# Kernel tuning notes

Measured on AMD Instinct MI355X. Metric: run time of the kernel, lower is better.

## Reference

```python
import jax, jax.numpy as jnp
import numpy as np

B, L, D, N, NL = 8, 32768, 64, 16, 4


def setup_inputs() -> dict:
    key = jax.random.key(0)
    ks = jax.random.split(key, 32)
    r = lambda i, shape, s=1.0: s * jax.random.normal(ks[i], shape, dtype=jnp.float32)
    return {
        "inputs": r(0, (B, L)),
        "w_init": r(1, (D, 1), 0.5), "b_init": r(2, (D,), 0.1),
        "s4_ln_w": 1.0 + r(3, (NL, D), 0.05), "s4_ln_b": r(4, (NL, D), 0.05),
        "log_dt": r(5, (NL, D), 0.5) - 4.0,          # dt ~ exp(-4) ~ 0.018
        "log_A_real": r(6, (NL, D, N), 0.3),
        "A_imag": r(7, (NL, D, N)),
        "C_re": r(8, (NL, D, N), 0.5), "C_im": r(9, (NL, D, N), 0.5),
        "D_skip": r(10, (NL, D)),
        "s4_out_w": r(11, (NL, 2 * D, D), 0.1), "s4_out_b": r(12, (NL, 2 * D), 0.05),
        "ff_ln_w": 1.0 + r(13, (NL, D), 0.05), "ff_ln_b": r(14, (NL, D), 0.05),
        "ff_w1": r(15, (NL, 2 * D, D), 0.1), "ff_b1": r(16, (NL, 2 * D), 0.05),
        "ff_w2": r(17, (NL, D, 2 * D), 0.1), "ff_b2": r(18, (NL, D), 0.05),
        "norm_w": 1.0 + r(19, (D,), 0.05), "norm_b": r(20, (D,), 0.05),
        "w_final1": r(21, (D, D), 0.1), "b_final1": r(22, (D,), 0.05),
        "w_zero": r(23, (1, D), 0.02), "b_zero": r(24, (1,), 0.01),
    }


def _ln(x, w, b):
    # layernorm over channel dim of [B, D, L] (TransposedLN)
    m = jnp.mean(x, axis=1, keepdims=True)
    v = jnp.var(x, axis=1, keepdims=True)
    return (x - m) * jax.lax.rsqrt(v + 1e-5) * w[None, :, None] + b[None, :, None]


def _s4d(z, log_dt, log_A_real, A_imag, C_re, C_im, D_skip):
    # S4D (diagonal SSM) with ZOH discretization; z: [B, D, L]
    Lq = z.shape[-1]
    dt = jnp.exp(log_dt)                              # [D]
    A = -jnp.exp(log_A_real) + 1j * A_imag            # [D, N]
    dtA = A * dt[:, None]                             # [D, N]
    C = (C_re + 1j * C_im) * (jnp.exp(dtA) - 1.0) / A # dC = C * (e^{dtA}-1)/A
    t = jnp.arange(Lq)
    # Vandermonde kernel K[d, l] = 2 Re sum_n dC[d,n] e^{dtA[d,n] * l}
    K = 2.0 * jnp.real(jnp.einsum('dn,dnl->dl', C, jnp.exp(dtA[:, :, None] * t)))
    n = 2 * Lq
    y = jnp.fft.irfft(jnp.fft.rfft(z, n) * jnp.fft.rfft(K, n)[None], n)[..., :Lq]
    return y + D_skip[None, :, None] * z


def reference(inputs, w_init, b_init, s4_ln_w, s4_ln_b, log_dt, log_A_real,
              A_imag, C_re, C_im, D_skip, s4_out_w, s4_out_b, ff_ln_w, ff_ln_b,
              ff_w1, ff_b1, ff_w2, ff_b2, norm_w, norm_b, w_final1, b_final1,
              w_zero, b_zero):
    # init conv (1x1) + ReLU; inputs [B, L] -> x [B, D, L]
    x = jax.nn.relu(jnp.einsum('dc,bcl->bdl', w_init, inputs[:, None, :])
                    + b_init[None, :, None])
    for i in range(NL):
        # --- S4 residual block: LN -> S4D -> GELU -> 1x1 conv to 2D -> GLU ---
        z = _ln(x, s4_ln_w[i], s4_ln_b[i])
        y = _s4d(z, log_dt[i], log_A_real[i], A_imag[i], C_re[i], C_im[i], D_skip[i])
        y = jax.nn.gelu(y)
        u = jnp.einsum('ed,bdl->bel', s4_out_w[i], y) + s4_out_b[i][None, :, None]
        a, g = jnp.split(u, 2, axis=1)
        x = x + a * jax.nn.sigmoid(g)
        z = _ln(x, ff_ln_w[i], ff_ln_b[i])
        h = jax.nn.gelu(jnp.einsum('ed,bdl->bel', ff_w1[i], z) + ff_b1[i][None, :, None])
        x = x + jnp.einsum('de,bel->bdl', ff_w2[i], h) + ff_b2[i][None, :, None]
    # final norm + conv head
    x = _ln(x, norm_w, norm_b)
    x = jax.nn.relu(jnp.einsum('ed,bdl->bel', w_final1, x) + b_final1[None, :, None])
    x = jnp.einsum('od,bdl->bol', w_zero, x) + b_zero[None, :, None]
    return x[:, 0, :]  # squeeze out_channels=1 -> [B, L]
```

## Files before the change

### kernel.cpp

```cpp
#include <hip/hip_runtime.h>
#include <cmath>

constexpr int Bq = 8, Lq = 32768, Dq = 64, Nq = 16, NLq = 4;
constexpr int CLq = 128, NCq = 256;
constexpr int PT = Bq * Lq / 16;

typedef _Float16 f16;
typedef _Float16 half2t __attribute__((ext_vector_type(2)));
typedef _Float16 half4 __attribute__((ext_vector_type(4)));
typedef _Float16 half8 __attribute__((ext_vector_type(8)));
typedef float f32x4 __attribute__((ext_vector_type(4)));
typedef float f32x2 __attribute__((ext_vector_type(2)));

static __device__ __forceinline__ float sigm(float x) { return 1.0f / (1.0f + __expf(-x)); }
static __device__ __forceinline__ float gelu_t(float x) {
  return x * sigm(1.5957691216057308f * fmaf(0.044715f * x * x, x, x));
}

__global__ __launch_bounds__(128) void k_wtall(
    const float* __restrict__ log_dt, const float* __restrict__ log_A_real,
    const float* __restrict__ A_imag, const float* __restrict__ C_re,
    const float* __restrict__ C_im, const float* __restrict__ dskip,
    f32x2* __restrict__ LCL, f32x2* __restrict__ LC2K, half8* __restrict__ TF,
    half8* __restrict__ VF, half8* __restrict__ WF) {
  __shared__ f32x2 pw[129][16];
  __shared__ f32x2 lamS[16], dcS[16];
  __shared__ float Ks[128];
  int d = blockIdx.x & 63, L = blockIdx.x >> 6;
  half8* TFl = TF + (size_t)L * 131072;
  half8* VFl = VF + (size_t)L * 32768;
  half8* WFl = WF + (size_t)L * 32768;
  int t = threadIdx.x;
  if (t < 16) {
    int di = L * 64 + d;
    int idx = di * 16 + t;
    float dt = expf(log_dt[di]);
    float Ar = -expf(log_A_real[idx]);
    float Ai = A_imag[idx];
    float dr = Ar * dt, dmi = Ai * dt;
    float er = expf(dr);
    float lr = er * cosf(dmi), li = er * sinf(dmi);
    float inv = 1.0f / (Ar * Ar + Ai * Ai);
    float e1r = lr - 1.0f, e1i = li;
    float qr = (e1r * Ar + e1i * Ai) * inv;
    float qi = (e1i * Ar - e1r * Ai) * inv;
    float cr = C_re[idx], ci = C_im[idx];
    lamS[t] = f32x2{lr, li};
    dcS[t] = f32x2{2.0f * (cr * qr - ci * qi), 2.0f * (cr * qi + ci * qr)};
    float erc = expf(dr * 128.0f);
    f32x2 l128 = f32x2{erc * cosf(dmi * 128.0f), erc * sinf(dmi * 128.0f)};
    pw[128][t] = l128;
    LCL[(size_t)L * 1024 + d * 16 + t] = l128;
    float br = l128.x, bi = l128.y;
#pragma unroll
    for (int q = 0; q < 4; q++) {
      float t2 = br * br - bi * bi;
      bi = 2.f * br * bi; br = t2;
    }
    LC2K[(size_t)L * 1024 + d * 16 + t] = f32x2{br, bi};
  }
  __syncthreads();
#pragma unroll
  for (int n = 0; n < 16; n++) {
    f32x2 lam = lamS[n];
    float pr = 1.f, pi = 0.f, br = lam.x, bi = lam.y;
    int e = t;
    while (e) {
      if (e & 1) { float tt = pr * br - pi * bi; pi = fmaf(pr, bi, pi * br); pr = tt; }
      float t2 = br * br - bi * bi; bi = 2.f * br * bi; br = t2; e >>= 1;
    }
    pw[t][n] = f32x2{pr, pi};
  }
  __syncthreads();
  {
    float k = 0.f;
#pragma unroll
    for (int n = 0; n < 16; n++) {
      f32x2 dc = dcS[n];
      f32x2 p = pw[t][n];
      k += dc.x * p.x - dc.y * p.y;
    }
    if (t == 0) k += dskip[L * 64 + d];
    Ks[t] = k;
  }
  __syncthreads();
  for (int s = t; s < 2048; s += 128) {
    int ln = s & 63, kt = (s >> 6) & 3, mt = s >> 8;
    int jo = mt * 16 + (ln & 15);
    int ji0 = kt * 32 + (ln >> 4) * 8;
    half8 v;
#pragma unroll
    for (int jj = 0; jj < 8; jj++) {
      int ji = ji0 + jj;
      v[jj] = (jo >= ji) ? (f16)Ks[jo - ji] : (f16)0.f;
    }
    TFl[(size_t)d * 2048 + s] = v;
  }
  for (int s = t; s < 512; s += 128) {
    int ln = s & 63, mt = s >> 6;
    int jo = mt * 16 + (ln & 15);
    int q0 = (ln >> 4) * 8;
    half8 v;
#pragma unroll
    for (int jj = 0; jj < 8; jj++) {
      int q = q0 + jj, n = q >> 1;
      f32x2 dc = dcS[n];
      f32x2 p = pw[jo + 1][n];
      float wr = dc.x * p.x - dc.y * p.y;
      float wi = dc.x * p.y + dc.y * p.x;
      v[jj] = (q & 1) ? (f16)(-wi) : (f16)wr;
    }
    VFl[(size_t)d * 512 + s] = v;
  }
  for (int s = t; s < 512; s += 128) {
    int ln = s & 63, kt = (s >> 6) & 3, nt = s >> 8;
    int p_ = nt * 16 + (ln & 15);
    int n = p_ >> 1;
    int j0 = kt * 32 + (ln >> 4) * 8;
    half8 v;
#pragma unroll
    for (int jj = 0; jj < 8; jj++) {
      f32x2 p = pw[127 - (j0 + jj)][n];
      v[jj] = (p_ & 1) ? (f16)p.y : (f16)p.x;
    }
    WFl[(size_t)d * 512 + s] = v;
  }
}

__global__ __launch_bounds__(512) void k_init3(
    const float* __restrict__ inp, const float* __restrict__ w_init,
    const float* __restrict__ b_init, const float* __restrict__ lnw,
    const float* __restrict__ lnb, f16* __restrict__ X, f16* __restrict__ Z16) {
  __shared__ __align__(16) f16 ztile[64 * 132];
  int tid = threadIdx.x;
  int widx = tid >> 6, lane = tid & 63;
  int pl = lane & 15, qh = lane >> 4;
  for (int k = 0; k < 4; ++k) {
    int pt = blockIdx.x * 8 + widx + k * 4096;
    int pos = pt * 16 + pl;
    float v = inp[pos];
    float s = 0.f, s2 = 0.f;
    f32x4 o[4];
#pragma unroll
    for (int q = 0; q < 4; q++) {
      int d0 = q * 16 + qh * 4;
      f32x4 w4 = *(const f32x4*)(w_init + d0);
      f32x4 b4 = *(const f32x4*)(b_init + d0);
#pragma unroll
      for (int j = 0; j < 4; j++) {
        float t = fmaf(w4[j], v, b4[j]);
        t = t > 0.f ? t : 0.f;
        o[q][j] = t; s += t; s2 += t * t;
      }
      half4 xo = half4{(f16)o[q][0], (f16)o[q][1], (f16)o[q][2], (f16)o[q][3]};
      *(half4*)(X + (size_t)pos * 64 + d0) = xo;
    }
    s += __shfl_xor(s, 16); s += __shfl_xor(s, 32);
    s2 += __shfl_xor(s2, 16); s2 += __shfl_xor(s2, 32);
    float m = s * (1.0f / 64.0f);
    float rstd = rsqrtf(s2 * (1.0f / 64.0f) - m * m + 1e-5f);
    int prow = widx * 16 + pl;
#pragma unroll
    for (int q = 0; q < 4; q++) {
      int d0 = q * 16 + qh * 4;
      f32x4 lw = *(const f32x4*)(lnw + d0);
      f32x4 lb = *(const f32x4*)(lnb + d0);
#pragma unroll
      for (int r = 0; r < 4; r++)
        ztile[(d0 + r) * 132 + prow] = (f16)fmaf((o[q][r] - m) * rstd, lw[r], lb[r]);
    }
    __syncthreads();
    {
      int d = tid >> 3, c0 = (tid & 7) * 16;
      half8 z0 = *(const half8*)(ztile + d * 132 + c0);
      half8 z1 = *(const half8*)(ztile + d * 132 + c0 + 8);
      size_t zoff = (size_t)d * 262144 + (size_t)(blockIdx.x * 8 + k * 4096) * 16;
      *(half8*)(Z16 + zoff + c0) = z0;
      *(half8*)(Z16 + zoff + c0 + 8) = z1;
    }
    __syncthreads();
  }
}

__global__ __launch_bounds__(256) void k_p1g(
    const f16* __restrict__ Z16, const half8* __restrict__ WF, f16* __restrict__ S16) {
  int tid = threadIdx.x;
  int lane = tid & 63;
  int task = blockIdx.x * 4 + (tid >> 6);
  int d = task >> 7, bct = task & 127;
  int bc0 = bct * 16;
  int pl = lane & 15, qh = lane >> 4;
  half8 az[4];
  const f16* zp = Z16 + ((size_t)d * 2048 + bc0 + pl) * 128 + qh * 8;
#pragma unroll
  for (int kt = 0; kt < 4; kt++) az[kt] = *(const half8*)(zp + kt * 32);
#pragma unroll
  for (int nt = 0; nt < 2; nt++) {
    f32x4 acc = f32x4{0.f, 0.f, 0.f, 0.f};
#pragma unroll
    for (int kt = 0; kt < 4; kt++)
      acc = __builtin_amdgcn_mfma_f32_16x16x32_f16(az[kt], WF[(size_t)d * 512 + (nt * 4 + kt) * 64 + lane], acc, 0, 0, 0);
#pragma unroll
    for (int r = 0; r < 4; r++)
      S16[((size_t)d * 2048 + bc0 + qh * 4 + r) * 32 + nt * 16 + pl] = (f16)acc[r];
  }
}

__global__ __launch_bounds__(256) void k_pass2(
    const f16* __restrict__ S16, const f32x2* __restrict__ LCLl,
    const f32x2* __restrict__ LC2Kl, f16* __restrict__ Sc) {
  __shared__ f32x2 gc[16][17];
  int blk = blockIdx.x;
  int d = blk >> 3, b = blk & 7;
  int t = threadIdx.x;
  int n = t & 15, g = t >> 4;
  f32x2 lam = LCLl[d * 16 + n];
  size_t base = ((size_t)d * 2048 + b * 256 + g * 16) * 32 + 2 * n;
  const f16* sp = S16 + base;
  float cr = 0.f, ci = 0.f;
#pragma unroll 4
  for (int j = 0; j < 16; j++) {
    half2t v = *(const half2t*)(sp + (size_t)j * 32);
    float nr = fmaf(lam.x, cr, fmaf(-lam.y, ci, (float)v[0]));
    float ni = fmaf(lam.x, ci, fmaf(lam.y, cr, (float)v[1]));
    cr = nr; ci = ni;
  }
  gc[g][n] = f32x2{cr, ci};
  __syncthreads();
  f32x2 l2 = LC2Kl[d * 16 + n];
  float er = 0.f, ei = 0.f;
  for (int gg = 0; gg < g; gg++) {
    f32x2 c = gc[gg][n];
    float nr = fmaf(l2.x, er, fmaf(-l2.y, ei, c.x));
    float ni = fmaf(l2.x, ei, fmaf(l2.y, er, c.y));
    er = nr; ei = ni;
  }
  f16* cp = Sc + base;
  float cr2 = er, ci2 = ei;
#pragma unroll 4
  for (int j = 0; j < 16; j++) {
    *(half2t*)(cp + (size_t)j * 32) = half2t{(f16)cr2, (f16)ci2};
    half2t v = *(const half2t*)(sp + (size_t)j * 32);
    float nr = fmaf(lam.x, cr2, fmaf(-lam.y, ci2, (float)v[0]));
    float ni = fmaf(lam.x, ci2, fmaf(lam.y, cr2, (float)v[1]));
    cr2 = nr; ci2 = ni;
  }
}

__global__ __launch_bounds__(256) void k_p3g2(
    const f16* __restrict__ Z16, const f16* __restrict__ Sc,
    const half8* __restrict__ TF, const half8* __restrict__ VF,
    f16* __restrict__ Y16) {
  int tid = threadIdx.x;
  int lane = tid & 63, widx = tid >> 6;
  int bct = blockIdx.x & 127, dg = blockIdx.x >> 7;
  int bc0 = bct * 16;
  int dbase = dg * 16 + widx * 4;
  int pl = lane & 15, qh = lane >> 4;
  half8 zb[4][4];
  half8 sb[4];
#pragma unroll
  for (int di = 0; di < 4; di++) {
    int d = dbase + di;
    const f16* zp = Z16 + ((size_t)d * 2048 + bc0 + pl) * 128 + qh * 8;
#pragma unroll
    for (int kt = 0; kt < 4; kt++) zb[di][kt] = *(const half8*)(zp + kt * 32);
    sb[di] = *(const half8*)(Sc + ((size_t)d * 2048 + bc0 + pl) * 32 + qh * 8);
  }
#pragma unroll
  for (int mt = 0; mt < 8; mt++) {
    const int KTM = mt / 2 + 1;
    f32x4 acc[4];
#pragma unroll
    for (int di = 0; di < 4; di++) {
      int d = dbase + di;
      acc[di] = f32x4{0.f, 0.f, 0.f, 0.f};
      const half8* tfp = TF + ((size_t)d * 8 + mt) * 256 + lane;
#pragma unroll
      for (int kt = 0; kt < KTM; kt++)
        acc[di] = __builtin_amdgcn_mfma_f32_16x16x32_f16(tfp[kt * 64], zb[di][kt], acc[di], 0, 0, 0);
      acc[di] = __builtin_amdgcn_mfma_f32_16x16x32_f16(VF[((size_t)d * 8 + mt) * 64 + lane], sb[di], acc[di], 0, 0, 0);
    }
#pragma unroll
    for (int r = 0; r < 4; r++) {
      int pos = (bc0 + pl) * 128 + mt * 16 + qh * 4 + r;
      half4 pk = half4{(f16)gelu_t(acc[0][r]), (f16)gelu_t(acc[1][r]),
                       (f16)gelu_t(acc[2][r]), (f16)gelu_t(acc[3][r])};
      *(half4*)(Y16 + (size_t)pos * 64 + dbase) = pk;
    }
  }
}

template <int WZ>
__global__ __launch_bounds__(512) void k_gluff3(
    const f16* __restrict__ Y16, const float* __restrict__ Wg, const float* __restrict__ bg,
    const float* __restrict__ W1, const float* __restrict__ b1,
    const float* __restrict__ W2, const float* __restrict__ b2,
    const float* __restrict__ lnw, const float* __restrict__ lnb,
    const float* __restrict__ nlnw, const float* __restrict__ nlnb,
    f16* __restrict__ X, f16* __restrict__ Z16,
    const float* __restrict__ Wf, const float* __restrict__ bfb,
    const float* __restrict__ wz, const float* __restrict__ bz,
    float* __restrict__ outp) {
  __shared__ __align__(16) char smem[68352];
  int tid = threadIdx.x;
#pragma unroll
  for (int it = 0; it < 2; it++) {
    int s = it * 512 + tid;
    int l = s & 63, ks = (s >> 6) & 1, et = s >> 7;
    const float* wp = Wg + (et * 16 + (l & 15)) * 64 + ks * 32 + (l >> 4) * 8;
    f32x4 w0 = *(const f32x4*)wp, w1 = *(const f32x4*)(wp + 4);
    *(half8*)(smem + s * 16) = half8{(f16)w0[0], (f16)w0[1], (f16)w0[2], (f16)w0[3],
                                     (f16)w1[0], (f16)w1[1], (f16)w1[2], (f16)w1[3]};
  }
#pragma unroll
  for (int it = 0; it < 2; it++) {
    int s = it * 512 + tid;
    int l = s & 63, ks = (s >> 6) & 1, et = s >> 7;
    int pls = l & 15, qhs = l >> 4;
    const float* wp = W1 + (et * 16 + pls) * 64 + ks * 32 + qhs * 4;
    f32x4 w0 = *(const f32x4*)wp;
    f32x4 w1 = *(const f32x4*)(wp + 16);
    *(half8*)(smem + 16384 + s * 16) = half8{(f16)w0[0], (f16)w0[1], (f16)w0[2], (f16)w0[3],
                                             (f16)w1[0], (f16)w1[1], (f16)w1[2], (f16)w1[3]};
  }
#pragma unroll
  for (int it = 0; it < 2; it++) {
    int s = it * 512 + tid;
    int l = s & 63, ks = (s >> 6) & 3, dt = s >> 8;
    int pls = l & 15, qhs = l >> 4;
    const float* wp = W2 + (dt * 16 + pls) * 128 + ks * 32 + qhs * 4;
    f32x4 w0 = *(const f32x4*)wp;
    f32x4 w1 = *(const f32x4*)(wp + 16);
    *(half8*)(smem + 32768 + s * 16) = half8{(f16)w0[0], (f16)w0[1], (f16)w0[2], (f16)w0[3],
                                             (f16)w1[0], (f16)w1[1], (f16)w1[2], (f16)w1[3]};
  }
  for (int idx = tid; idx < 576; idx += 512) {
    float v;
    if (idx < 128) v = bg[idx];
    else if (idx < 256) v = b1[idx - 128];
    else if (idx < 320) v = b2[idx - 256];
    else if (idx < 384) v = lnw[idx - 320];
    else if (idx < 448) v = lnb[idx - 384];
    else if (idx < 512) v = nlnw[idx - 448];
    else v = nlnb[idx - 512];
    ((float*)(smem + 49152))[idx] = v;
  }
  if constexpr (!WZ) {
    if (tid < 512) {
      int s = tid;
      int l = s & 63, ks = (s >> 6) & 1, et = s >> 7;
      int pls = l & 15, qhs = l >> 4;
      const float* wp = Wf + (et * 16 + pls) * 64 + ks * 32 + qhs * 4;
      f32x4 w0 = *(const f32x4*)wp;
      f32x4 w1 = *(const f32x4*)(wp + 16);
      *(half8*)(smem + 51456 + s * 16) = half8{(f16)w0[0], (f16)w0[1], (f16)w0[2], (f16)w0[3],
                                               (f16)w1[0], (f16)w1[1], (f16)w1[2], (f16)w1[3]};
    }
    if (tid < 129) {
      float v = tid < 64 ? bfb[tid] : (tid < 128 ? wz[tid - 64] : bz[0]);
      ((float*)(smem + 59648))[tid] = v;
    }
  }
  __syncthreads();
  int lane = tid & 63, pl = lane & 15, qh = lane >> 4;
  int widx = tid >> 6;
  f16* ztile = (f16*)(smem + 51456);

  for (int k = 0; k < 4; ++k) {
    int pt = blockIdx.x * 8 + widx + k * 4096;
    int pos = pt * 16 + pl;
    half8 yb0 = *(const half8*)(Y16 + (size_t)pos * 64 + qh * 8);
    half8 yb1 = *(const half8*)(Y16 + (size_t)pos * 64 + 32 + qh * 8);
    f32x4 xv[4];
#pragma unroll
    for (int q = 0; q < 4; q++) {
      half4 xh = *(const half4*)(X + (size_t)pos * 64 + q * 16 + qh * 4);
#pragma unroll
      for (int r = 0; r < 4; r++) xv[q][r] = (float)xh[r];
    }

    unsigned sb = 0;
    asm volatile("" : "+v"(sb));
    const char* sm = smem + sb;
    const half8* sWg = (const half8*)sm;
    const half8* sW1 = (const half8*)(sm + 16384);
    const half8* sW2 = (const half8*)(sm + 32768);
    const float* sf = (const float*)(sm + 49152);
    f32x4 accg[8];
#pragma unroll
    for (int et = 0; et < 8; et++) accg[et] = *(const f32x4*)(sf + et * 16 + qh * 4);
#pragma unroll
    for (int et = 0; et < 8; et++)
      accg[et] = __builtin_amdgcn_mfma_f32_16x16x32_f16(sWg[(et * 2) * 64 + lane], yb0, accg[et], 0, 0, 0);
#pragma unroll
    for (int et = 0; et < 8; et++)
      accg[et] = __builtin_amdgcn_mfma_f32_16x16x32_f16(sWg[(et * 2 + 1) * 64 + lane], yb1, accg[et], 0, 0, 0);
    float s = 0.f, s2 = 0.f;
#pragma unroll
    for (int q = 0; q < 4; q++)
#pragma unroll
      for (int r = 0; r < 4; r++) {
        xv[q][r] += accg[q][r] * sigm(accg[q + 4][r]);
        s += xv[q][r]; s2 += xv[q][r] * xv[q][r];
      }
    s += __shfl_xor(s, 16); s += __shfl_xor(s, 32);
    s2 += __shfl_xor(s2, 16); s2 += __shfl_xor(s2, 32);
    float m = s * (1.0f / 64.0f);
    float rstd = rsqrtf(s2 * (1.0f / 64.0f) - m * m + 1e-5f);
    half4 zb4[4];
#pragma unroll
    for (int ks = 0; ks < 4; ks++) {
      f32x4 lw = *(const f32x4*)(sf + 320 + ks * 16 + qh * 4);
      f32x4 lb = *(const f32x4*)(sf + 384 + ks * 16 + qh * 4);
      half4 z;
#pragma unroll
      for (int r = 0; r < 4; r++) z[r] = (f16)fmaf((xv[ks][r] - m) * rstd, lw[r], lb[r]);
      zb4[ks] = z;
    }
    f32x4 acc1[8];
#pragma unroll
    for (int et = 0; et < 8; et++) acc1[et] = *(const f32x4*)(sf + 128 + et * 16 + qh * 4);
#pragma unroll
    for (int ks = 0; ks < 2; ks++) {
      half4 a = zb4[ks * 2], b = zb4[ks * 2 + 1];
      half8 zb8 = half8{a[0], a[1], a[2], a[3], b[0], b[1], b[2], b[3]};
#pragma unroll
      for (int et = 0; et < 8; et++)
        acc1[et] = __builtin_amdgcn_mfma_f32_16x16x32_f16(sW1[(et * 2 + ks) * 64 + lane], zb8, acc1[et], 0, 0, 0);
    }
    half4 h4[8];
#pragma unroll
    for (int et = 0; et < 8; et++)
      h4[et] = half4{(f16)gelu_t(acc1[et][0]), (f16)gelu_t(acc1[et][1]),
                     (f16)gelu_t(acc1[et][2]), (f16)gelu_t(acc1[et][3])};
    f32x4 acc2[4];
#pragma unroll
    for (int dt = 0; dt < 4; dt++) acc2[dt] = *(const f32x4*)(sf + 256 + dt * 16 + qh * 4);
#pragma unroll
    for (int ks = 0; ks < 4; ks++) {
      half4 a = h4[ks * 2], b = h4[ks * 2 + 1];
      half8 hb8 = half8{a[0], a[1], a[2], a[3], b[0], b[1], b[2], b[3]};
#pragma unroll
      for (int dt = 0; dt < 4; dt++)
        acc2[dt] = __builtin_amdgcn_mfma_f32_16x16x32_f16(sW2[(dt * 4 + ks) * 64 + lane], hb8, acc2[dt], 0, 0, 0);
    }
    s = 0.f; s2 = 0.f;
#pragma unroll
    for (int dt = 0; dt < 4; dt++) {
#pragma unroll
      for (int r = 0; r < 4; r++) {
        xv[dt][r] += acc2[dt][r];
        s += xv[dt][r]; s2 += xv[dt][r] * xv[dt][r];
      }
      if constexpr (WZ) {
        half4 xo = half4{(f16)xv[dt][0], (f16)xv[dt][1], (f16)xv[dt][2], (f16)xv[dt][3]};
        *(half4*)(X + (size_t)pos * 64 + dt * 16 + qh * 4) = xo;
      }
    }
    s += __shfl_xor(s, 16); s += __shfl_xor(s, 32);
    s2 += __shfl_xor(s2, 16); s2 += __shfl_xor(s2, 32);
    float m2 = s * (1.0f / 64.0f);
    float rstd2 = rsqrtf(s2 * (1.0f / 64.0f) - m2 * m2 + 1e-5f);

    if constexpr (WZ) {
      int prow = widx * 16 + pl;
#pragma unroll
      for (int q = 0; q < 4; q++) {
        int d0 = q * 16 + qh * 4;
        f32x4 lw = *(const f32x4*)(sf + 448 + d0);
        f32x4 lb = *(const f32x4*)(sf + 512 + d0);
#pragma unroll
        for (int r = 0; r < 4; r++)
          ztile[(d0 + r) * 132 + prow] = (f16)fmaf((xv[q][r] - m2) * rstd2, lw[r], lb[r]);
      }
      __syncthreads();
      {
        int d = tid >> 3, c0 = (tid & 7) * 16;
        half8 z0 = *(const half8*)(ztile + d * 132 + c0);
        half8 z1 = *(const half8*)(ztile + d * 132 + c0 + 8);
        size_t zoff = (size_t)d * 262144 + (size_t)(blockIdx.x * 8 + k * 4096) * 16;
        *(half8*)(Z16 + zoff + c0) = z0;
        *(half8*)(Z16 + zoff + c0 + 8) = z1;
      }
      __syncthreads();
    } else {
      const half8* sWf = (const half8*)(sm + 51456);
      const float* hf = (const float*)(sm + 59648);
      half4 hz[4];
#pragma unroll
      for (int ks = 0; ks < 4; ks++) {
        f32x4 lw = *(const f32x4*)(sf + 448 + ks * 16 + qh * 4);
        f32x4 lb = *(const f32x4*)(sf + 512 + ks * 16 + qh * 4);
        half4 z;
#pragma unroll
        for (int r = 0; r < 4; r++) z[r] = (f16)fmaf((xv[ks][r] - m2) * rstd2, lw[r], lb[r]);
        hz[ks] = z;
      }
      f32x4 acch[4];
#pragma unroll
      for (int et = 0; et < 4; et++) acch[et] = *(const f32x4*)(hf + et * 16 + qh * 4);
#pragma unroll
      for (int ks = 0; ks < 2; ks++) {
        half4 a = hz[ks * 2], b = hz[ks * 2 + 1];
        half8 zb8 = half8{a[0], a[1], a[2], a[3], b[0], b[1], b[2], b[3]};
#pragma unroll
        for (int et = 0; et < 4; et++)
          acch[et] = __builtin_amdgcn_mfma_f32_16x16x32_f16(sWf[(et * 2 + ks) * 64 + lane], zb8, acch[et], 0, 0, 0);
      }
      float o = 0.f;
#pragma unroll
      for (int et = 0; et < 4; et++) {
        f32x4 wzv = *(const f32x4*)(hf + 64 + et * 16 + qh * 4);
#pragma unroll
        for (int r = 0; r < 4; r++) {
          float rv = acch[et][r];
          rv = rv > 0.f ? rv : 0.f;
          o = fmaf(wzv[r], rv, o);
        }
      }
      o += __shfl_xor(o, 16); o += __shfl_xor(o, 32);
      if (qh == 0) outp[pos] = o + hf[128];
    }
  }
}

extern "C" void kernel_launch(void* const* d_in, const int* in_sizes, int n_in,
                              void* d_out, int out_size, void* d_ws, size_t ws_size,
                              hipStream_t stream) {
  (void)in_sizes; (void)n_in; (void)out_size; (void)ws_size;
  const float* inputs   = (const float*)d_in[0];
  const float* w_init   = (const float*)d_in[1];
  const float* b_init   = (const float*)d_in[2];
  const float* s4_ln_w  = (const float*)d_in[3];
  const float* s4_ln_b  = (const float*)d_in[4];
  const float* log_dt   = (const float*)d_in[5];
  const float* log_A    = (const float*)d_in[6];
  const float* A_imag   = (const float*)d_in[7];
  const float* C_re     = (const float*)d_in[8];
  const float* C_im     = (const float*)d_in[9];
  const float* D_skip   = (const float*)d_in[10];
  const float* s4_out_w = (const float*)d_in[11];
  const float* s4_out_b = (const float*)d_in[12];
  const float* ff_ln_w  = (const float*)d_in[13];
  const float* ff_ln_b  = (const float*)d_in[14];
  const float* ff_w1    = (const float*)d_in[15];
  const float* ff_b1    = (const float*)d_in[16];
  const float* ff_w2    = (const float*)d_in[17];
  const float* ff_b2    = (const float*)d_in[18];
  const float* norm_w   = (const float*)d_in[19];
  const float* norm_b   = (const float*)d_in[20];
  const float* w_final1 = (const float*)d_in[21];
  const float* b_final1 = (const float*)d_in[22];
  const float* w_zero   = (const float*)d_in[23];
  const float* b_zero   = (const float*)d_in[24];

  char* w8 = (char*)d_ws;
  size_t off = 0;
  f16*   X     = (f16*)(w8 + off);   off += (size_t)33554432;
  f16*   Z16   = (f16*)(w8 + off);   off += (size_t)33554432;
  f16*   Y16   = (f16*)(w8 + off);   off += (size_t)33554432;
  f16*   S16   = (f16*)(w8 + off);   off += (size_t)8388608;
  f16*   Sc    = (f16*)(w8 + off);   off += (size_t)8388608;
  f32x2* LCL   = (f32x2*)(w8 + off); off += 32768;
  f32x2* LC2K  = (f32x2*)(w8 + off); off += 32768;
  half8* TF    = (half8*)(w8 + off); off += (size_t)8388608;
  half8* VF    = (half8*)(w8 + off); off += (size_t)2097152;
  half8* WF    = (half8*)(w8 + off); off += (size_t)2097152;

  k_wtall<<<256, 128, 0, stream>>>(log_dt, log_A, A_imag, C_re, C_im, D_skip,
                                   LCL, LC2K, TF, VF, WF);
  k_init3<<<512, 512, 0, stream>>>(inputs, w_init, b_init, s4_ln_w, s4_ln_b, X, Z16);
  for (int i = 0; i < NLq; i++) {
    k_p1g<<<2048, 256, 0, stream>>>(Z16, WF + (size_t)i * 32768, S16);
    k_pass2<<<512, 256, 0, stream>>>(S16, LCL + i * 1024, LC2K + i * 1024, Sc);
    k_p3g2<<<512, 256, 0, stream>>>(Z16, Sc, TF + (size_t)i * 131072, VF + (size_t)i * 32768, Y16);
    if (i < NLq - 1) {
      k_gluff3<1><<<512, 512, 0, stream>>>(Y16, s4_out_w + i * 8192, s4_out_b + i * 128,
                                           ff_w1 + i * 8192, ff_b1 + i * 128,
                                           ff_w2 + i * 8192, ff_b2 + i * 64,
                                           ff_ln_w + i * 64, ff_ln_b + i * 64,
                                           s4_ln_w + (i + 1) * 64, s4_ln_b + (i + 1) * 64,
                                           X, Z16, nullptr, nullptr, nullptr, nullptr, nullptr);
    } else {
      k_gluff3<0><<<512, 512, 0, stream>>>(Y16, s4_out_w + i * 8192, s4_out_b + i * 128,
                                           ff_w1 + i * 8192, ff_b1 + i * 128,
                                           ff_w2 + i * 8192, ff_b2 + i * 64,
                                           ff_ln_w + i * 64, ff_ln_b + i * 64,
                                           norm_w, norm_b,
                                           X, Z16, w_final1, b_final1, w_zero, b_zero,
                                           (float*)d_out);
    }
  }
}
```

Baseline: 457.1 us.

## Split p3g2 into two triangular halves and widen gluff to 1024-thread blocks

The chunked convolution kernel is split so that each block handles half of the output tiles, either the first four or the last four. The first half loads only the Z fragments its triangular structure needs, and the grid doubles to give more parallel blocks. The GLU/FF kernel now runs 1024 threads per block, each warp doing two iterations instead of four. The transposed Z tile is written back in two synchronised rounds through the same shared buffer. This is meant to raise occupancy and parallelism, at the cost of extra barriers and uneven work between the two halves.

```diff
diff --git a/kernel.cpp b/kernel.cpp
--- a/kernel.cpp
+++ b/kernel.cpp
@@ -247,52 +247,65 @@
   }
 }
 
+template <int NKT, int MT0>
+__device__ __forceinline__ void p3g2_body(
+    const f16* __restrict__ Z16, const f16* __restrict__ Sc,
+    const half8* __restrict__ TF, const half8* __restrict__ VF,
+    f16* __restrict__ Y16, int bc0, int dbase, int lane, int pl, int qh) {
+  half8 zb[4][NKT];
+  half8 sb[4];
+#pragma unroll
+  for (int di = 0; di < 4; di++) {
+    int d = dbase + di;
+    const f16* zp = Z16 + ((size_t)d * 2048 + bc0 + pl) * 128 + qh * 8;
+#pragma unroll
+    for (int kt = 0; kt < NKT; kt++) zb[di][kt] = *(const half8*)(zp + kt * 32);
+    sb[di] = *(const half8*)(Sc + ((size_t)d * 2048 + bc0 + pl) * 32 + qh * 8);
+  }
+#pragma unroll
+  for (int u = 0; u < 4; u++) {
+    const int mt = MT0 + u;
+    const int KTM = mt / 2 + 1;
+    f32x4 acc[4];
+#pragma unroll
+    for (int di = 0; di < 4; di++) {
+      int d = dbase + di;
+      acc[di] = f32x4{0.f, 0.f, 0.f, 0.f};
+      const half8* tfp = TF + ((size_t)d * 8 + mt) * 256 + lane;
+#pragma unroll
+      for (int kt = 0; kt < KTM; kt++)
+        acc[di] = __builtin_amdgcn_mfma_f32_16x16x32_f16(tfp[kt * 64], zb[di][kt], acc[di], 0, 0, 0);
+      acc[di] = __builtin_amdgcn_mfma_f32_16x16x32_f16(VF[((size_t)d * 8 + mt) * 64 + lane], sb[di], acc[di], 0, 0, 0);
+    }
+#pragma unroll
+    for (int r = 0; r < 4; r++) {
+      int pos = (bc0 + pl) * 128 + mt * 16 + qh * 4 + r;
+      half4 pk = half4{(f16)gelu_t(acc[0][r]), (f16)gelu_t(acc[1][r]),
+                       (f16)gelu_t(acc[2][r]), (f16)gelu_t(acc[3][r])};
+      *(half4*)(Y16 + (size_t)pos * 64 + dbase) = pk;
+    }
+  }
+}
+
 __global__ __launch_bounds__(256) void k_p3g2(
     const f16* __restrict__ Z16, const f16* __restrict__ Sc,
     const half8* __restrict__ TF, const half8* __restrict__ VF,
     f16* __restrict__ Y16) {
   int tid = threadIdx.x;
   int lane = tid & 63, widx = tid >> 6;
-  int bct = blockIdx.x & 127, dg = blockIdx.x >> 7;
+  int blk = blockIdx.x;
+  int half = blk >> 9, dg = (blk >> 7) & 3, bct = blk & 127;
   int bc0 = bct * 16;
   int dbase = dg * 16 + widx * 4;
   int pl = lane & 15, qh = lane >> 4;
-  half8 zb[4][4];
-  half8 sb[4];
-#pragma unroll
-  for (int di = 0; di < 4; di++) {
-    int d = dbase + di;
-    const f16* zp = Z16 + ((size_t)d * 2048 + bc0 + pl) * 128 + qh * 8;
-#pragma unroll
-    for (int kt = 0; kt < 4; kt++) zb[di][kt] = *(const half8*)(zp + kt * 32);
-    sb[di] = *(const half8*)(Sc + ((size_t)d * 2048 + bc0 + pl) * 32 + qh * 8);
-  }
-#pragma unroll
-  for (int mt = 0; mt < 8; mt++) {
-    const int KTM = mt / 2 + 1;
-    f32x4 acc[4];
-#pragma unroll
-    for (int di = 0; di < 4; di++) {
-      int d = dbase + di;
-      acc[di] = f32x4{0.f, 0.f, 0.f, 0.f};
-      const half8* tfp = TF + ((size_t)d * 8 + mt) * 256 + lane;
-#pragma unroll
-      for (int kt = 0; kt < KTM; kt++)
-        acc[di] = __builtin_amdgcn_mfma_f32_16x16x32_f16(tfp[kt * 64], zb[di][kt], acc[di], 0, 0, 0);
-      acc[di] = __builtin_amdgcn_mfma_f32_16x16x32_f16(VF[((size_t)d * 8 + mt) * 64 + lane], sb[di], acc[di], 0, 0, 0);
-    }
-#pragma unroll
-    for (int r = 0; r < 4; r++) {
-      int pos = (bc0 + pl) * 128 + mt * 16 + qh * 4 + r;
-      half4 pk = half4{(f16)gelu_t(acc[0][r]), (f16)gelu_t(acc[1][r]),
-                       (f16)gelu_t(acc[2][r]), (f16)gelu_t(acc[3][r])};
-      *(half4*)(Y16 + (size_t)pos * 64 + dbase) = pk;
-    }
-  }
+  if (half == 0)
+    p3g2_body<2, 0>(Z16, Sc, TF, VF, Y16, bc0, dbase, lane, pl, qh);
+  else
+    p3g2_body<4, 4>(Z16, Sc, TF, VF, Y16, bc0, dbase, lane, pl, qh);
 }
 
 template <int WZ>
-__global__ __launch_bounds__(512) void k_gluff3(
+__global__ __launch_bounds__(1024, 8) void k_gluff4(
     const f16* __restrict__ Y16, const float* __restrict__ Wg, const float* __restrict__ bg,
     const float* __restrict__ W1, const float* __restrict__ b1,
     const float* __restrict__ W2, const float* __restrict__ b2,
@@ -304,18 +317,16 @@
     float* __restrict__ outp) {
   __shared__ __align__(16) char smem[68352];
   int tid = threadIdx.x;
-#pragma unroll
-  for (int it = 0; it < 2; it++) {
-    int s = it * 512 + tid;
+  {
+    int s = tid;
     int l = s & 63, ks = (s >> 6) & 1, et = s >> 7;
     const float* wp = Wg + (et * 16 + (l & 15)) * 64 + ks * 32 + (l >> 4) * 8;
     f32x4 w0 = *(const f32x4*)wp, w1 = *(const f32x4*)(wp + 4);
     *(half8*)(smem + s * 16) = half8{(f16)w0[0], (f16)w0[1], (f16)w0[2], (f16)w0[3],
                                      (f16)w1[0], (f16)w1[1], (f16)w1[2], (f16)w1[3]};
   }
-#pragma unroll
-  for (int it = 0; it < 2; it++) {
-    int s = it * 512 + tid;
+  {
+    int s = tid;
     int l = s & 63, ks = (s >> 6) & 1, et = s >> 7;
     int pls = l & 15, qhs = l >> 4;
     const float* wp = W1 + (et * 16 + pls) * 64 + ks * 32 + qhs * 4;
@@ -324,9 +335,8 @@
     *(half8*)(smem + 16384 + s * 16) = half8{(f16)w0[0], (f16)w0[1], (f16)w0[2], (f16)w0[3],
                                              (f16)w1[0], (f16)w1[1], (f16)w1[2], (f16)w1[3]};
   }
-#pragma unroll
-  for (int it = 0; it < 2; it++) {
-    int s = it * 512 + tid;
+  {
+    int s = tid;
     int l = s & 63, ks = (s >> 6) & 3, dt = s >> 8;
     int pls = l & 15, qhs = l >> 4;
     const float* wp = W2 + (dt * 16 + pls) * 128 + ks * 32 + qhs * 4;
@@ -335,7 +345,8 @@
     *(half8*)(smem + 32768 + s * 16) = half8{(f16)w0[0], (f16)w0[1], (f16)w0[2], (f16)w0[3],
                                              (f16)w1[0], (f16)w1[1], (f16)w1[2], (f16)w1[3]};
   }
-  for (int idx = tid; idx < 576; idx += 512) {
+  if (tid < 576) {
+    int idx = tid;
     float v;
     if (idx < 128) v = bg[idx];
     else if (idx < 256) v = b1[idx - 128];
@@ -367,8 +378,8 @@
   int widx = tid >> 6;
   f16* ztile = (f16*)(smem + 51456);
 
-  for (int k = 0; k < 4; ++k) {
-    int pt = blockIdx.x * 8 + widx + k * 4096;
+  for (int k = 0; k < 2; ++k) {
+    int pt = blockIdx.x * 16 + widx + k * 8192;
     int pos = pt * 16 + pl;
     half8 yb0 = *(const half8*)(Y16 + (size_t)pos * 64 + qh * 8);
     half8 yb1 = *(const half8*)(Y16 + (size_t)pos * 64 + 32 + qh * 8);
@@ -464,24 +475,48 @@
     float rstd2 = rsqrtf(s2 * (1.0f / 64.0f) - m2 * m2 + 1e-5f);
 
     if constexpr (WZ) {
-      int prow = widx * 16 + pl;
+      half4 zreg[4];
 #pragma unroll
       for (int q = 0; q < 4; q++) {
         int d0 = q * 16 + qh * 4;
         f32x4 lw = *(const f32x4*)(sf + 448 + d0);
         f32x4 lb = *(const f32x4*)(sf + 512 + d0);
-#pragma unroll
-        for (int r = 0; r < 4; r++)
-          ztile[(d0 + r) * 132 + prow] = (f16)fmaf((xv[q][r] - m2) * rstd2, lw[r], lb[r]);
+        half4 z;
+#pragma unroll
+        for (int r = 0; r < 4; r++) z[r] = (f16)fmaf((xv[q][r] - m2) * rstd2, lw[r], lb[r]);
+        zreg[q] = z;
+      }
+      size_t baseA = (size_t)blockIdx.x * 256 + (size_t)k * 131072;
+      if (widx < 8) {
+        int prow = widx * 16 + pl;
+#pragma unroll
+        for (int q = 0; q < 4; q++) {
+          int d0 = q * 16 + qh * 4;
+#pragma unroll
+          for (int r = 0; r < 4; r++) ztile[(d0 + r) * 132 + prow] = zreg[q][r];
+        }
       }
       __syncthreads();
       {
-        int d = tid >> 3, c0 = (tid & 7) * 16;
+        int d = tid >> 4, c0 = (tid & 15) * 8;
         half8 z0 = *(const half8*)(ztile + d * 132 + c0);
-        half8 z1 = *(const half8*)(ztile + d * 132 + c0 + 8);
-        size_t zoff = (size_t)d * 262144 + (size_t)(blockIdx.x * 8 + k * 4096) * 16;
-        *(half8*)(Z16 + zoff + c0) = z0;
-        *(half8*)(Z16 + zoff + c0 + 8) = z1;
+        *(half8*)(Z16 + (size_t)d * 262144 + baseA + c0) = z0;
+      }
+      __syncthreads();
+      if (widx >= 8) {
+        int prow = (widx - 8) * 16 + pl;
+#pragma unroll
+        for (int q = 0; q < 4; q++) {
+          int d0 = q * 16 + qh * 4;
+#pragma unroll
+          for (int r = 0; r < 4; r++) ztile[(d0 + r) * 132 + prow] = zreg[q][r];
+        }
+      }
+      __syncthreads();
+      {
+        int d = tid >> 4, c0 = (tid & 15) * 8;
+        half8 z0 = *(const half8*)(ztile + d * 132 + c0);
+        *(half8*)(Z16 + (size_t)d * 262144 + baseA + 128 + c0) = z0;
       }
       __syncthreads();
     } else {
@@ -574,22 +609,22 @@
   for (int i = 0; i < NLq; i++) {
     k_p1g<<<2048, 256, 0, stream>>>(Z16, WF + (size_t)i * 32768, S16);
     k_pass2<<<512, 256, 0, stream>>>(S16, LCL + i * 1024, LC2K + i * 1024, Sc);
-    k_p3g2<<<512, 256, 0, stream>>>(Z16, Sc, TF + (size_t)i * 131072, VF + (size_t)i * 32768, Y16);
+    k_p3g2<<<1024, 256, 0, stream>>>(Z16, Sc, TF + (size_t)i * 131072, VF + (size_t)i * 32768, Y16);
     if (i < NLq - 1) {
-      k_gluff3<1><<<512, 512, 0, stream>>>(Y16, s4_out_w + i * 8192, s4_out_b + i * 128,
-                                           ff_w1 + i * 8192, ff_b1 + i * 128,
-                                           ff_w2 + i * 8192, ff_b2 + i * 64,
-                                           ff_ln_w + i * 64, ff_ln_b + i * 64,
-                                           s4_ln_w + (i + 1) * 64, s4_ln_b + (i + 1) * 64,
-                                           X, Z16, nullptr, nullptr, nullptr, nullptr, nullptr);
+      k_gluff4<1><<<512, 1024, 0, stream>>>(Y16, s4_out_w + i * 8192, s4_out_b + i * 128,
+                                            ff_w1 + i * 8192, ff_b1 + i * 128,
+                                            ff_w2 + i * 8192, ff_b2 + i * 64,
+                                            ff_ln_w + i * 64, ff_ln_b + i * 64,
+                                            s4_ln_w + (i + 1) * 64, s4_ln_b + (i + 1) * 64,
+                                            X, Z16, nullptr, nullptr, nullptr, nullptr, nullptr);
     } else {
-      k_gluff3<0><<<512, 512, 0, stream>>>(Y16, s4_out_w + i * 8192, s4_out_b + i * 128,
-                                           ff_w1 + i * 8192, ff_b1 + i * 128,
-                                           ff_w2 + i * 8192, ff_b2 + i * 64,
-                                           ff_ln_w + i * 64, ff_ln_b + i * 64,
-                                           norm_w, norm_b,
-                                           X, Z16, w_final1, b_final1, w_zero, b_zero,
-                                           (float*)d_out);
-    }
-  }
-}
+      k_gluff4<0><<<512, 1024, 0, stream>>>(Y16, s4_out_w + i * 8192, s4_out_b + i * 128,
+                                            ff_w1 + i * 8192, ff_b1 + i * 128,
+                                            ff_w2 + i * 8192, ff_b2 + i * 64,
+                                            ff_ln_w + i * 64, ff_ln_b + i * 64,
+                                            norm_w, norm_b,
+                                            X, Z16, w_final1, b_final1, w_zero, b_zero,
+                                            (float*)d_out);
+    }
+  }
+}
```

New measurement: 538.6 us. 17.8% more time.

## Move FF W2 weights from LDS to pre-swizzled global, raise gluff occupancy

Applied to the files above, without the earlier changes.

Adds a one-time prep kernel that converts each layer's FF W2 weights to fp16 in MFMA fragment order in global memory, so the GLU/FF kernel reads them directly from global/L2 instead of staging them in LDS. This cuts shared memory per block from about 67KB to about 51KB. The kernel also gets a launch-bounds occupancy hint and a grid of 768 blocks with a strided tile loop, aiming for more resident work per CU. The cost is extra global/L2 traffic for the W2 fragments inside the inner loop, plus a tail imbalance because 2048 tiles per block-row do not divide evenly by 768 blocks.

```diff
diff --git a/kernel.cpp b/kernel.cpp
--- a/kernel.cpp
+++ b/kernel.cpp
@@ -127,6 +127,25 @@
   }
 }
 
+__global__ __launch_bounds__(256) void k_wprep(
+    const float* __restrict__ W2all, half8* __restrict__ W2F) {
+  int L = blockIdx.x;
+  const float* W2 = W2all + L * 8192;
+  half8* out = W2F + (size_t)L * 1024;
+  int tid = threadIdx.x;
+#pragma unroll
+  for (int it = 0; it < 4; it++) {
+    int s = it * 256 + tid;
+    int l = s & 63, ks = (s >> 6) & 3, dt = s >> 8;
+    int pls = l & 15, qhs = l >> 4;
+    const float* wp = W2 + (dt * 16 + pls) * 128 + ks * 32 + qhs * 4;
+    f32x4 w0 = *(const f32x4*)wp;
+    f32x4 w1 = *(const f32x4*)(wp + 16);
+    out[s] = half8{(f16)w0[0], (f16)w0[1], (f16)w0[2], (f16)w0[3],
+                   (f16)w1[0], (f16)w1[1], (f16)w1[2], (f16)w1[3]};
+  }
+}
+
 __global__ __launch_bounds__(512) void k_init3(
     const float* __restrict__ inp, const float* __restrict__ w_init,
     const float* __restrict__ b_init, const float* __restrict__ lnw,
@@ -292,17 +311,17 @@
 }
 
 template <int WZ>
-__global__ __launch_bounds__(512) void k_gluff3(
+__global__ __launch_bounds__(512, 6) void k_gluff5(
     const f16* __restrict__ Y16, const float* __restrict__ Wg, const float* __restrict__ bg,
     const float* __restrict__ W1, const float* __restrict__ b1,
-    const float* __restrict__ W2, const float* __restrict__ b2,
+    const half8* __restrict__ W2F, const float* __restrict__ b2,
     const float* __restrict__ lnw, const float* __restrict__ lnb,
     const float* __restrict__ nlnw, const float* __restrict__ nlnb,
     f16* __restrict__ X, f16* __restrict__ Z16,
     const float* __restrict__ Wf, const float* __restrict__ bfb,
     const float* __restrict__ wz, const float* __restrict__ bz,
     float* __restrict__ outp) {
-  __shared__ __align__(16) char smem[68352];
+  __shared__ __align__(16) char smem[51968];
   int tid = threadIdx.x;
 #pragma unroll
   for (int it = 0; it < 2; it++) {
@@ -324,17 +343,6 @@
     *(half8*)(smem + 16384 + s * 16) = half8{(f16)w0[0], (f16)w0[1], (f16)w0[2], (f16)w0[3],
                                              (f16)w1[0], (f16)w1[1], (f16)w1[2], (f16)w1[3]};
   }
-#pragma unroll
-  for (int it = 0; it < 2; it++) {
-    int s = it * 512 + tid;
-    int l = s & 63, ks = (s >> 6) & 3, dt = s >> 8;
-    int pls = l & 15, qhs = l >> 4;
-    const float* wp = W2 + (dt * 16 + pls) * 128 + ks * 32 + qhs * 4;
-    f32x4 w0 = *(const f32x4*)wp;
-    f32x4 w1 = *(const f32x4*)(wp + 16);
-    *(half8*)(smem + 32768 + s * 16) = half8{(f16)w0[0], (f16)w0[1], (f16)w0[2], (f16)w0[3],
-                                             (f16)w1[0], (f16)w1[1], (f16)w1[2], (f16)w1[3]};
-  }
   for (int idx = tid; idx < 576; idx += 512) {
     float v;
     if (idx < 128) v = bg[idx];
@@ -344,7 +352,7 @@
     else if (idx < 448) v = lnb[idx - 384];
     else if (idx < 512) v = nlnw[idx - 448];
     else v = nlnb[idx - 512];
-    ((float*)(smem + 49152))[idx] = v;
+    ((float*)(smem + 32768))[idx] = v;
   }
   if constexpr (!WZ) {
     if (tid < 512) {
@@ -354,21 +362,21 @@
       const float* wp = Wf + (et * 16 + pls) * 64 + ks * 32 + qhs * 4;
       f32x4 w0 = *(const f32x4*)wp;
       f32x4 w1 = *(const f32x4*)(wp + 16);
-      *(half8*)(smem + 51456 + s * 16) = half8{(f16)w0[0], (f16)w0[1], (f16)w0[2], (f16)w0[3],
+      *(half8*)(smem + 35072 + s * 16) = half8{(f16)w0[0], (f16)w0[1], (f16)w0[2], (f16)w0[3],
                                                (f16)w1[0], (f16)w1[1], (f16)w1[2], (f16)w1[3]};
     }
     if (tid < 129) {
       float v = tid < 64 ? bfb[tid] : (tid < 128 ? wz[tid - 64] : bz[0]);
-      ((float*)(smem + 59648))[tid] = v;
+      ((float*)(smem + 43264))[tid] = v;
     }
   }
   __syncthreads();
   int lane = tid & 63, pl = lane & 15, qh = lane >> 4;
   int widx = tid >> 6;
-  f16* ztile = (f16*)(smem + 51456);
-
-  for (int k = 0; k < 4; ++k) {
-    int pt = blockIdx.x * 8 + widx + k * 4096;
+  f16* ztile = (f16*)(smem + 35072);
+
+  for (int pt0 = blockIdx.x * 8; pt0 < PT; pt0 += 6144) {
+    int pt = pt0 + widx;
     int pos = pt * 16 + pl;
     half8 yb0 = *(const half8*)(Y16 + (size_t)pos * 64 + qh * 8);
     half8 yb1 = *(const half8*)(Y16 + (size_t)pos * 64 + 32 + qh * 8);
@@ -380,13 +388,14 @@
       for (int r = 0; r < 4; r++) xv[q][r] = (float)xh[r];
     }
 
-    unsigned sb = 0;
+    unsigned sb = 0, o2 = 0;
     asm volatile("" : "+v"(sb));
+    asm volatile("" : "+v"(o2));
     const char* sm = smem + sb;
     const half8* sWg = (const half8*)sm;
     const half8* sW1 = (const half8*)(sm + 16384);
-    const half8* sW2 = (const half8*)(sm + 32768);
-    const float* sf = (const float*)(sm + 49152);
+    const half8* sW2g = W2F + o2;
+    const float* sf = (const float*)(sm + 32768);
     f32x4 accg[8];
 #pragma unroll
     for (int et = 0; et < 8; et++) accg[et] = *(const f32x4*)(sf + et * 16 + qh * 4);
@@ -443,7 +452,7 @@
       half8 hb8 = half8{a[0], a[1], a[2], a[3], b[0], b[1], b[2], b[3]};
 #pragma unroll
       for (int dt = 0; dt < 4; dt++)
-        acc2[dt] = __builtin_amdgcn_mfma_f32_16x16x32_f16(sW2[(dt * 4 + ks) * 64 + lane], hb8, acc2[dt], 0, 0, 0);
+        acc2[dt] = __builtin_amdgcn_mfma_f32_16x16x32_f16(sW2g[(dt * 4 + ks) * 64 + lane], hb8, acc2[dt], 0, 0, 0);
     }
     s = 0.f; s2 = 0.f;
 #pragma unroll
@@ -479,14 +488,14 @@
         int d = tid >> 3, c0 = (tid & 7) * 16;
         half8 z0 = *(const half8*)(ztile + d * 132 + c0);
         half8 z1 = *(const half8*)(ztile + d * 132 + c0 + 8);
-        size_t zoff = (size_t)d * 262144 + (size_t)(blockIdx.x * 8 + k * 4096) * 16;
+        size_t zoff = (size_t)d * 262144 + (size_t)pt0 * 16;
         *(half8*)(Z16 + zoff + c0) = z0;
         *(half8*)(Z16 + zoff + c0 + 8) = z1;
       }
       __syncthreads();
     } else {
-      const half8* sWf = (const half8*)(sm + 51456);
-      const float* hf = (const float*)(sm + 59648);
+      const half8* sWf = (const half8*)(sm + 35072);
+      const float* hf = (const float*)(sm + 43264);
       half4 hz[4];
 #pragma unroll
       for (int ks = 0; ks < 4; ks++) {
@@ -567,25 +576,27 @@
   half8* TF    = (half8*)(w8 + off); off += (size_t)8388608;
   half8* VF    = (half8*)(w8 + off); off += (size_t)2097152;
   half8* WF    = (half8*)(w8 + off); off += (size_t)2097152;
+  half8* W2F   = (half8*)(w8 + off); off += 65536;
 
   k_wtall<<<256, 128, 0, stream>>>(log_dt, log_A, A_imag, C_re, C_im, D_skip,
                                    LCL, LC2K, TF, VF, WF);
+  k_wprep<<<4, 256, 0, stream>>>(ff_w2, W2F);
   k_init3<<<512, 512, 0, stream>>>(inputs, w_init, b_init, s4_ln_w, s4_ln_b, X, Z16);
   for (int i = 0; i < NLq; i++) {
     k_p1g<<<2048, 256, 0, stream>>>(Z16, WF + (size_t)i * 32768, S16);
     k_pass2<<<512, 256, 0, stream>>>(S16, LCL + i * 1024, LC2K + i * 1024, Sc);
     k_p3g2<<<512, 256, 0, stream>>>(Z16, Sc, TF + (size_t)i * 131072, VF + (size_t)i * 32768, Y16);
     if (i < NLq - 1) {
-      k_gluff3<1><<<512, 512, 0, stream>>>(Y16, s4_out_w + i * 8192, s4_out_b + i * 128,
+      k_gluff5<1><<<768, 512, 0, stream>>>(Y16, s4_out_w + i * 8192, s4_out_b + i * 128,
                                            ff_w1 + i * 8192, ff_b1 + i * 128,
-                                           ff_w2 + i * 8192, ff_b2 + i * 64,
+                                           W2F + (size_t)i * 1024, ff_b2 + i * 64,
                                            ff_ln_w + i * 64, ff_ln_b + i * 64,
                                            s4_ln_w + (i + 1) * 64, s4_ln_b + (i + 1) * 64,
                                            X, Z16, nullptr, nullptr, nullptr, nullptr, nullptr);
     } else {
-      k_gluff3<0><<<512, 512, 0, stream>>>(Y16, s4_out_w + i * 8192, s4_out_b + i * 128,
+      k_gluff5<0><<<768, 512, 0, stream>>>(Y16, s4_out_w + i * 8192, s4_out_b + i * 128,
                                            ff_w1 + i * 8192, ff_b1 + i * 128,
-                                           ff_w2 + i * 8192, ff_b2 + i * 64,
+                                           W2F + (size_t)i * 1024, ff_b2 + i * 64,
                                            ff_ln_w + i * 64, ff_ln_b + i * 64,
                                            norm_w, norm_b,
                                            X, Z16, w_final1, b_final1, w_zero, b_zero,
```

Result: slower. 509.5 us (+11.5%).
